# Optimization experiments

Measured on AMD Instinct MI355X. Metric: run time of the kernel, lower is better.

The kernel has to match this reference:

```python
import jax, jax.numpy as jnp
import numpy as np
import math

D_MODEL = 768
H = 12
D_FF = 3072
HEAD_DIM = D_MODEL // H
EPS = 1e-5


def setup_inputs() -> dict:
    key = jax.random.key(0)
    ks = jax.random.split(key, 12)
    s = 1.0 / math.sqrt(D_MODEL)
    inp = {
        "x": jax.random.normal(ks[0], (8, 1024, D_MODEL), dtype=jnp.float32),
        # attention projections (stored as [d_in, d_out])
        "wq": jax.random.normal(ks[1], (D_MODEL, D_MODEL), jnp.float32) * s,
        "bq": jnp.zeros((D_MODEL,), jnp.float32),
        "wk": jax.random.normal(ks[2], (D_MODEL, D_MODEL), jnp.float32) * s,
        "bk": jnp.zeros((D_MODEL,), jnp.float32),
        "wv": jax.random.normal(ks[3], (D_MODEL, D_MODEL), jnp.float32) * s,
        "bv": jnp.zeros((D_MODEL,), jnp.float32),
        "wo": jax.random.normal(ks[4], (D_MODEL, D_MODEL), jnp.float32) * s,
        "bo": jnp.zeros((D_MODEL,), jnp.float32),
        # FFN
        "w1": jax.random.normal(ks[5], (D_MODEL, D_FF), jnp.float32) * s,
        "b1": jnp.zeros((D_FF,), jnp.float32),
        "w2": jax.random.normal(ks[6], (D_FF, D_MODEL), jnp.float32) * (1.0 / math.sqrt(D_FF)),
        "b2": jnp.zeros((D_MODEL,), jnp.float32),
        # LayerNormalization scalar params (gemma/beta) for the two residual norms
        "g1": jnp.ones((1,), jnp.float32),
        "be1": jnp.zeros((1,), jnp.float32),
        "g2": jnp.ones((1,), jnp.float32),
        "be2": jnp.zeros((1,), jnp.float32),
    }
    return inp


def _layernorm(x, g, b):
    # torch: mean and UNBIASED std over last dim; divide by (std + eps)
    mean = jnp.mean(x, axis=-1, keepdims=True)
    std = jnp.std(x, axis=-1, keepdims=True, ddof=1)
    return g * (x - mean) / (std + EPS) + b


def _attention(x, wq, bq, wk, bk, wv, bv, wo, bo):
    B, N, _ = x.shape
    q = (x @ wq + bq).reshape(B, N, H, HEAD_DIM)
    k = (x @ wk + bk).reshape(B, N, H, HEAD_DIM)
    v = (x @ wv + bv).reshape(B, N, H, HEAD_DIM)
    scores = jnp.einsum("bqhd,bkhd->bhqk", q, k) / math.sqrt(HEAD_DIM)
    w = jax.nn.softmax(scores, axis=-1)
    out = jnp.einsum("bhqk,bkhd->bqhd", w, v).reshape(B, N, D_MODEL)
    return out @ wo + bo


def _ffn(x, w1, b1, w2, b2):
    return (jax.nn.gelu(x @ w1 + b1, approximate=False)) @ w2 + b2


def reference(x, wq, bq, wk, bk, wv, bv, wo, bo, w1, b1, w2, b2, g1, be1, g2, be2):
    # pre-LN residual block 1: attention
    x = x + _attention(_layernorm(x, g1, be1), wq, bq, wk, bk, wv, bv, wo, bo)
    # pre-LN residual block 2: FFN
    x = x + _ffn(_layernorm(x, g2, be2), w1, b1, w2, b2)
    return x
```

## Files before the change

### kernel.cpp

```cpp
#include <hip/hip_runtime.h>
#include <hip/hip_bf16.h>
#include <math.h>

typedef unsigned short u16;
typedef unsigned int u32;
typedef u16 u16x8 __attribute__((ext_vector_type(8)));
typedef __bf16 bf16x8 __attribute__((ext_vector_type(8)));
typedef float f32x4 __attribute__((ext_vector_type(4)));

#define MODE_GELU 1
#define MODE_RESF32 2
#define MODE_QKV 3

template <typename T, typename F>
__device__ __forceinline__ T bitcast(F f) { return __builtin_bit_cast(T, f); }

__device__ __forceinline__ u16 f2bf(float f) {
    unsigned int u = __float_as_uint(f);
    u = (u + 0x7fffu + ((u >> 16) & 1u)) >> 16;
    return (u16)u;
}

__device__ __forceinline__ u32 packbf(float lo, float hi) {
    return (u32)f2bf(lo) | ((u32)f2bf(hi) << 16);
}

__device__ __forceinline__ float fast_gelu(float x) {
    const float arg = x * (2.30220775f + 0.10294329f * x * x);
    const float e = exp2f(arg);
    return x * (1.0f - __builtin_amdgcn_rcpf(e + 1.0f));
}

__device__ __forceinline__ void gl_lds16(const u16* g, u16* l) {
    __builtin_amdgcn_global_load_lds(
        (const __attribute__((address_space(1))) unsigned int*)(const void*)g,
        (__attribute__((address_space(3))) unsigned int*)(void*)l,
        16, 0, 0);
}

__device__ __forceinline__ void stage64(const u16* __restrict__ src, int stride,
                                        u16* __restrict__ lds, int t)
{
    const int wave = t >> 6, lane = t & 63;
#pragma unroll
    for (int i = 0; i < 2; i++) {
        const int row = i * 32 + wave * 8 + (lane >> 3);
        const int s = lane & 7;
        const int f = (((row >> 3) & 1) << 2) | (row & 3);
        gl_lds16(src + (size_t)row * stride + (size_t)((s ^ f) << 3),
                 lds + i * 2048 + wave * 512);
    }
}

__global__ __launch_bounds__(256) void prep_kernel(
    const float* __restrict__ wq, const float* __restrict__ wk,
    const float* __restrict__ wv, const float* __restrict__ wo,
    const float* __restrict__ w1, const float* __restrict__ w2,
    const float* __restrict__ bq, const float* __restrict__ bk,
    const float* __restrict__ bv,
    u16* __restrict__ wqkvT, u16* __restrict__ woT,
    u16* __restrict__ w1T, u16* __restrict__ w2T, float* __restrict__ bqkv)
{
    const int blk = blockIdx.x;
    if (blk >= 6912) {
        const int t = (blk - 6912) * 256 + threadIdx.x;
        if (t < 2304)
            bqkv[t] = t < 768 ? bq[t] : (t < 1536 ? bk[t - 768] : bv[t - 1536]);
        return;
    }
    const float* W; u16* WT; int Krows, Ncols, lt;
    if (blk < 576)       { W = wq; WT = wqkvT;                       Krows = 768;  Ncols = 768;  lt = blk; }
    else if (blk < 1152) { W = wk; WT = wqkvT + (size_t)768 * 768;   Krows = 768;  Ncols = 768;  lt = blk - 576; }
    else if (blk < 1728) { W = wv; WT = wqkvT + (size_t)1536 * 768;  Krows = 768;  Ncols = 768;  lt = blk - 1152; }
    else if (blk < 2304) { W = wo; WT = woT;                         Krows = 768;  Ncols = 768;  lt = blk - 1728; }
    else if (blk < 4608) { W = w1; WT = w1T;                         Krows = 768;  Ncols = 3072; lt = blk - 2304; }
    else                 { W = w2; WT = w2T;                         Krows = 3072; Ncols = 768;  lt = blk - 4608; }
    const int ktiles = Krows >> 5;
    const int k0 = (lt % ktiles) * 32, n0 = (lt / ktiles) * 32;

    __shared__ float tile[32][33];
    const int tx = threadIdx.x & 31, ty = threadIdx.x >> 5;
#pragma unroll
    for (int j = 0; j < 32; j += 8)
        tile[ty + j][tx] = W[(size_t)(k0 + ty + j) * Ncols + n0 + tx];
    __syncthreads();
#pragma unroll
    for (int j = 0; j < 32; j += 8)
        WT[(size_t)(n0 + ty + j) * Krows + k0 + tx] = f2bf(tile[tx][ty + j]);
}

__global__ __launch_bounds__(256) void ln_kernel(
    const float* __restrict__ X, u16* __restrict__ Y,
    const float* __restrict__ gp, const float* __restrict__ bp)
{
    __shared__ float sbuf[8];
    const int row = blockIdx.x, t = threadIdx.x;
    const float* xr = X + (size_t)row * 768;
    float v0 = xr[t], v1 = xr[t + 256], v2 = xr[t + 512];
    float s = v0 + v1 + v2;
    float q = v0 * v0 + v1 * v1 + v2 * v2;
#pragma unroll
    for (int m = 1; m < 64; m <<= 1) {
        s += __shfl_xor(s, m, 64);
        q += __shfl_xor(q, m, 64);
    }
    const int wave = t >> 6, lane = t & 63;
    if (lane == 0) { sbuf[wave] = s; sbuf[4 + wave] = q; }
    __syncthreads();
    s = sbuf[0] + sbuf[1] + sbuf[2] + sbuf[3];
    q = sbuf[4] + sbuf[5] + sbuf[6] + sbuf[7];
    const float mean = s * (1.0f / 768.0f);
    float ssd = q - 768.0f * mean * mean;
    ssd = fmaxf(ssd, 0.0f);
    const float stdv = sqrtf(ssd * (1.0f / 767.0f));
    const float scale = gp[0] / (stdv + 1e-5f);
    const float beta = bp[0];
    u16* yr = Y + (size_t)row * 768;
    yr[t]       = f2bf((v0 - mean) * scale + beta);
    yr[t + 256] = f2bf((v1 - mean) * scale + beta);
    yr[t + 512] = f2bf((v2 - mean) * scale + beta);
}

template <int MODE>
__global__ __launch_bounds__(256) void gemm_kernel(
    const u16* __restrict__ A, const u16* __restrict__ BT,
    const float* __restrict__ bias, const float* __restrict__ res,
    void* __restrict__ out0, void* __restrict__ out1, void* __restrict__ out2,
    int M, int N, int K)
{
    __shared__ u16 sh[2][2][128 * 64];
    u16* shp = &sh[0][0][0];
    const int t = threadIdx.x;
    const int lane = t & 63, wave = t >> 6;
    const int wr = wave >> 1, wc = wave & 1;
    const int g = lane >> 4, c = lane & 15;
    const int bm = blockIdx.x, bn = blockIdx.y;

    const int srow = wave * 32 + (lane >> 3);
    const int scol = (lane & 7) * 8;
    const u16* Ag = A + (size_t)(bm * 128 + srow) * K + scol;
    const u16* Bg = BT + (size_t)(bn * 128 + srow) * K + scol;

    f32x4 acc[4][4] = {};
    const int nk = K >> 6;

#define STAGE_AB(buf, k0)                                                     \
    {                                                                         \
        _Pragma("unroll")                                                     \
        for (int it = 0; it < 4; it++) {                                      \
            gl_lds16(Ag + (size_t)(it * 8) * K + (k0), &sh[buf][0][wave * 2048 + it * 512]); \
            gl_lds16(Bg + (size_t)(it * 8) * K + (k0), &sh[buf][1][wave * 2048 + it * 512]); \
        }                                                                     \
    }

    STAGE_AB(0, 0);
    __syncthreads();

    for (int ks = 0; ks < nk; ks++) {
        const int cur = ks & 1;
        if (ks + 1 < nk) STAGE_AB(cur ^ 1, (ks + 1) << 6);
        const u16* Asb = sh[cur][0];
        const u16* Bsb = sh[cur][1];
        __builtin_amdgcn_s_setprio(1);
#pragma unroll
        for (int kk = 0; kk < 2; kk++) {
            bf16x8 af[4], bfr[4];
#pragma unroll
            for (int m = 0; m < 4; m++)
                af[m] = *(const bf16x8*)&Asb[(wr * 64 + m * 16 + c) * 64 + kk * 32 + g * 8];
#pragma unroll
            for (int n = 0; n < 4; n++)
                bfr[n] = *(const bf16x8*)&Bsb[(wc * 64 + n * 16 + c) * 64 + kk * 32 + g * 8];
#pragma unroll
            for (int m = 0; m < 4; m++)
#pragma unroll
                for (int n = 0; n < 4; n++)
                    acc[m][n] = __builtin_amdgcn_mfma_f32_16x16x32_bf16(
                        af[m], bfr[n], acc[m][n], 0, 0, 0);
        }
        __builtin_amdgcn_s_setprio(0);
        __syncthreads();
    }
#undef STAGE_AB

    if constexpr (MODE == MODE_QKV) {
        if (bn >= 12) {
#pragma unroll
            for (int m = 0; m < 4; m++) {
#pragma unroll
                for (int n = 0; n < 4; n++) {
                    const int colL = wc * 64 + n * 16 + c;
                    const int rowLb = wr * 64 + m * 16 + 4 * g;
                    const float bv = bias[bn * 128 + colL];
                    const u32 x0 = packbf(acc[m][n][0] + bv, acc[m][n][1] + bv);
                    const u32 x1 = packbf(acc[m][n][2] + bv, acc[m][n][3] + bv);
                    const int elem = colL * 128 + (rowLb ^ ((colL & 15) << 3));
                    ((u32*)shp)[elem >> 1] = x0;
                    ((u32*)shp)[(elem >> 1) + 1] = x1;
                }
            }
            __syncthreads();
            const int bn_off = bn - 12;
            const int bb = bm >> 3, kvb = (bm & 7) * 128;
            const int j8 = (t & 7) * 8;
#pragma unroll
            for (int it = 0; it < 4; it++) {
                const int colL2 = it * 32 + (t >> 3);
                const int gcol = bn_off * 128 + colL2;
                const int hh = gcol >> 6, d = gcol & 63;
                const size_t obase = ((size_t)(bb * 12 + hh) << 16) + ((size_t)d << 10) + kvb;
                const int X = (colL2 & 15) << 3;
#pragma unroll
                for (int half = 0; half < 2; half++) {
                    const int rowL2 = half * 64 + j8;
                    const int elem = colL2 * 128 + (rowL2 ^ X);
                    *(u16x8*)((u16*)out2 + obase + rowL2) = *(const u16x8*)&shp[elem];
                }
            }
            return;
        }
    }

#pragma unroll
    for (int m = 0; m < 4; m++) {
        const int row = bm * 128 + wr * 64 + m * 16 + 4 * g;
#pragma unroll
        for (int n = 0; n < 4; n++) {
            const int col = bn * 128 + wc * 64 + n * 16 + c;
            const float bv = bias[col];
#pragma unroll
            for (int i = 0; i < 4; i++) {
                float v = acc[m][n][i] + bv;
                if constexpr (MODE == MODE_GELU) {
                    ((u16*)out0)[(size_t)(row + i) * N + col] = f2bf(fast_gelu(v));
                } else if constexpr (MODE == MODE_RESF32) {
                    const size_t idx = (size_t)(row + i) * N + col;
                    ((float*)out0)[idx] = v + res[idx];
                } else {
                    const int sect = (col >= 768) ? 1 : 0;
                    const int colm = col - sect * 768;
                    u16* dst = sect ? (u16*)out1 : (u16*)out0;
                    dst[(size_t)(row + i) * 768 + colm] = f2bf(v);
                }
            }
        }
    }
}

__global__ __launch_bounds__(256) void attn_kernel(
    const u16* __restrict__ Qg, const u16* __restrict__ Kg,
    const u16* __restrict__ Vt_g, u16* __restrict__ O)
{
    __shared__ u16 Kl[2][4096];
    __shared__ u16 Vl[2][4096];
    const int t = threadIdx.x, lane = t & 63, wave = t >> 6;
    const int g = lane >> 4, c = lane & 15;
    const int l = blockIdx.x;
    const int pos = l >> 3;
    const int bh = (l & 7) * 12 + (pos >> 3);
    const int qt = pos & 7;
    const int b = bh / 12, h = bh % 12;
    const size_t rowb = (size_t)b * 1024;
    const int q0 = qt * 128 + wave * 32;

    bf16x8 qa[2], qb[2];
    {
        const u16* qp = Qg + (rowb + q0 + c) * 768 + h * 64 + g * 8;
        u16x8 a0 = *(const u16x8*)qp;
        u16x8 a1 = *(const u16x8*)(qp + 32);
        u16x8 b0 = *(const u16x8*)(qp + 16 * 768);
        u16x8 b1 = *(const u16x8*)(qp + 16 * 768 + 32);
        bf16x8 va0, va1, vb0, vb1;
#pragma unroll
        for (int j = 0; j < 8; j++) {
            const float SC = 0.18033688011112042f;
            va0[j] = (__bf16)(__uint_as_float(((u32)a0[j]) << 16) * SC);
            va1[j] = (__bf16)(__uint_as_float(((u32)a1[j]) << 16) * SC);
            vb0[j] = (__bf16)(__uint_as_float(((u32)b0[j]) << 16) * SC);
            vb1[j] = (__bf16)(__uint_as_float(((u32)b1[j]) << 16) * SC);
        }
        qa[0] = va0; qa[1] = va1; qb[0] = vb0; qb[1] = vb1;
    }

    int kro[4], kxo[4], vro[4];
#pragma unroll
    for (int n = 0; n < 4; n++) {
        const int pr = ((n >> 1) << 5) + ((c >> 2) << 3) + ((n & 1) << 2) + (c & 3);
        kro[n] = pr << 6;
        kxo[n] = (((pr >> 3) & 1) << 2) | (pr & 3);
        vro[n] = (n * 16 + c) << 6;
    }
    const int vxo = (((c >> 3) & 1) << 2) | (c & 3);

    const u16* ksrc = Kg + rowb * 768 + h * 64;
    const u16* vsrc = Vt_g + (size_t)bh * 65536;

    float m0 = -1e30f, l0 = 0.f, m1 = -1e30f, l1 = 0.f;
    f32x4 oa[4] = {}, ob[4] = {};
    const int srcb = (lane & 48) | ((lane >> 2) & 12);

    stage64(ksrc, 768, Kl[0], t);
    stage64(vsrc, 1024, Vl[0], t);
    __syncthreads();

    for (int kvt = 0; kvt < 16; ++kvt) {
        const u16* Kc = Kl[kvt & 1];
        const u16* Vc = Vl[kvt & 1];
        if (kvt < 15) {
            stage64(ksrc + (size_t)(kvt + 1) * 64 * 768, 768, Kl[(kvt + 1) & 1], t);
            stage64(vsrc + (kvt + 1) * 64, 1024, Vl[(kvt + 1) & 1], t);
        }

        f32x4 s0[4] = {}, s1[4] = {};
#pragma unroll
        for (int n = 0; n < 4; n++) {
#pragma unroll
            for (int kk = 0; kk < 2; kk++) {
                const bf16x8 kf = *(const bf16x8*)&Kc[kro[n] + ((((kk << 2) + g) ^ kxo[n]) << 3)];
                s0[n] = __builtin_amdgcn_mfma_f32_16x16x32_bf16(kf, qa[kk], s0[n], 0, 0, 0);
                s1[n] = __builtin_amdgcn_mfma_f32_16x16x32_bf16(kf, qb[kk], s1[n], 0, 0, 0);
            }
        }

        bf16x8 pa00, pa01;
        {
            float t0 = fmaxf(fmaxf(s0[0][0], s0[0][1]), fmaxf(s0[0][2], s0[0][3]));
            float t1 = fmaxf(fmaxf(s0[1][0], s0[1][1]), fmaxf(s0[1][2], s0[1][3]));
            float t2 = fmaxf(fmaxf(s0[2][0], s0[2][1]), fmaxf(s0[2][2], s0[2][3]));
            float t3 = fmaxf(fmaxf(s0[3][0], s0[3][1]), fmaxf(s0[3][2], s0[3][3]));
            float mx = fmaxf(fmaxf(t0, t1), fmaxf(t2, t3));
            mx = fmaxf(mx, __shfl_xor(mx, 16, 64));
            mx = fmaxf(mx, __shfl_xor(mx, 32, 64));
            if (!__all(mx <= m0 + 8.0f)) {
                const float mn = fmaxf(m0, mx);
                const float rsc = exp2f(m0 - mn);
                m0 = mn; l0 *= rsc;
                f32x4 rq;
#pragma unroll
                for (int i = 0; i < 4; i++) rq[i] = __shfl(rsc, srcb + i, 64);
#pragma unroll
                for (int n = 0; n < 4; n++) oa[n] *= rq;
            }
            float r = 0.f;
#pragma unroll
            for (int n = 0; n < 4; n++)
#pragma unroll
                for (int i = 0; i < 4; i++) {
                    s0[n][i] = exp2f(s0[n][i] - m0);
                    r += s0[n][i];
                }
            r += __shfl_xor(r, 16, 64);
            r += __shfl_xor(r, 32, 64);
            l0 += r;
#pragma unroll
            for (int i = 0; i < 4; i++) {
                pa00[i] = (__bf16)s0[0][i]; pa00[4 + i] = (__bf16)s0[1][i];
                pa01[i] = (__bf16)s0[2][i]; pa01[4 + i] = (__bf16)s0[3][i];
            }
        }
        bf16x8 pa10, pa11;
        {
            float t0 = fmaxf(fmaxf(s1[0][0], s1[0][1]), fmaxf(s1[0][2], s1[0][3]));
            float t1 = fmaxf(fmaxf(s1[1][0], s1[1][1]), fmaxf(s1[1][2], s1[1][3]));
            float t2 = fmaxf(fmaxf(s1[2][0], s1[2][1]), fmaxf(s1[2][2], s1[2][3]));
            float t3 = fmaxf(fmaxf(s1[3][0], s1[3][1]), fmaxf(s1[3][2], s1[3][3]));
            float mx = fmaxf(fmaxf(t0, t1), fmaxf(t2, t3));
            mx = fmaxf(mx, __shfl_xor(mx, 16, 64));
            mx = fmaxf(mx, __shfl_xor(mx, 32, 64));
            if (!__all(mx <= m1 + 8.0f)) {
                const float mn = fmaxf(m1, mx);
                const float rsc = exp2f(m1 - mn);
                m1 = mn; l1 *= rsc;
                f32x4 rq;
#pragma unroll
                for (int i = 0; i < 4; i++) rq[i] = __shfl(rsc, srcb + i, 64);
#pragma unroll
                for (int n = 0; n < 4; n++) ob[n] *= rq;
            }
            float r = 0.f;
#pragma unroll
            for (int n = 0; n < 4; n++)
#pragma unroll
                for (int i = 0; i < 4; i++) {
                    s1[n][i] = exp2f(s1[n][i] - m1);
                    r += s1[n][i];
                }
            r += __shfl_xor(r, 16, 64);
            r += __shfl_xor(r, 32, 64);
            l1 += r;
#pragma unroll
            for (int i = 0; i < 4; i++) {
                pa10[i] = (__bf16)s1[0][i]; pa10[4 + i] = (__bf16)s1[1][i];
                pa11[i] = (__bf16)s1[2][i]; pa11[4 + i] = (__bf16)s1[3][i];
            }
        }

#pragma unroll
        for (int n = 0; n < 4; n++) {
#pragma unroll
            for (int kk = 0; kk < 2; kk++) {
                const bf16x8 vf = *(const bf16x8*)&Vc[vro[n] + ((((kk << 2) + g) ^ vxo) << 3)];
                oa[n] = __builtin_amdgcn_mfma_f32_16x16x32_bf16(kk ? pa01 : pa00, vf, oa[n], 0, 0, 0);
                ob[n] = __builtin_amdgcn_mfma_f32_16x16x32_bf16(kk ? pa11 : pa10, vf, ob[n], 0, 0, 0);
            }
        }
        __syncthreads();
    }

#pragma unroll
    for (int i = 0; i < 4; i++) {
        const float la = __shfl(l0, srcb + i, 64);
        const float lb = __shfl(l1, srcb + i, 64);
        const float ia_ = 1.0f / fmaxf(la, 1e-30f);
        const float ib_ = 1.0f / fmaxf(lb, 1e-30f);
        const size_t ra_ = rowb + q0 + 4 * g + i;
#pragma unroll
        for (int n = 0; n < 4; n++) {
            O[ra_ * 768 + h * 64 + n * 16 + c]        = f2bf(oa[n][i] * ia_);
            O[(ra_ + 16) * 768 + h * 64 + n * 16 + c] = f2bf(ob[n][i] * ib_);
        }
    }
}

extern "C" void kernel_launch(void* const* d_in, const int* in_sizes, int n_in,
                              void* d_out, int out_size, void* d_ws, size_t ws_size,
                              hipStream_t stream)
{
    const float* x   = (const float*)d_in[0];
    const float* wq  = (const float*)d_in[1];
    const float* bq  = (const float*)d_in[2];
    const float* wk  = (const float*)d_in[3];
    const float* bk  = (const float*)d_in[4];
    const float* wv  = (const float*)d_in[5];
    const float* bv  = (const float*)d_in[6];
    const float* wo  = (const float*)d_in[7];
    const float* bo  = (const float*)d_in[8];
    const float* w1  = (const float*)d_in[9];
    const float* b1  = (const float*)d_in[10];
    const float* w2  = (const float*)d_in[11];
    const float* b2  = (const float*)d_in[12];
    const float* g1  = (const float*)d_in[13];
    const float* be1 = (const float*)d_in[14];
    const float* g2  = (const float*)d_in[15];
    const float* be2 = (const float*)d_in[16];

    char* ws = (char*)d_ws;
    constexpr size_t O_WQKV = 0;
    constexpr size_t O_WO   = 3538944;
    constexpr size_t O_W1   = 4718592;
    constexpr size_t O_W2   = 9437184;
    constexpr size_t O_BQKV = 14155776;
    constexpr size_t O_XLN  = 14168064;
    constexpr size_t O_Q    = O_XLN + 12582912;
    constexpr size_t O_K    = O_Q + 12582912;
    constexpr size_t O_VT   = O_K + 12582912;
    constexpr size_t O_ATTN = O_VT + 12582912;
    constexpr size_t O_H    = O_ATTN + 12582912;
    constexpr size_t O_F    = O_XLN;
    constexpr size_t O_HLN  = O_ATTN;

    u16* wqkvT = (u16*)(ws + O_WQKV);
    u16* woT   = (u16*)(ws + O_WO);
    u16* w1T   = (u16*)(ws + O_W1);
    u16* w2T   = (u16*)(ws + O_W2);
    float* bqkv = (float*)(ws + O_BQKV);
    u16* xln   = (u16*)(ws + O_XLN);
    u16* Qb    = (u16*)(ws + O_Q);
    u16* Kb    = (u16*)(ws + O_K);
    u16* VTg   = (u16*)(ws + O_VT);
    u16* attnb = (u16*)(ws + O_ATTN);
    float* h   = (float*)(ws + O_H);
    u16* fb    = (u16*)(ws + O_F);
    u16* hln   = (u16*)(ws + O_HLN);

    dim3 blk(256);
    prep_kernel<<<6921, blk, 0, stream>>>(wq, wk, wv, wo, w1, w2, bq, bk, bv,
                                          wqkvT, woT, w1T, w2T, bqkv);
    ln_kernel<<<8192, blk, 0, stream>>>(x, xln, g1, be1);
    gemm_kernel<MODE_QKV><<<dim3(64, 18), blk, 0, stream>>>(
        xln, wqkvT, bqkv, nullptr, Qb, Kb, VTg, 8192, 2304, 768);
    attn_kernel<<<768, blk, 0, stream>>>(Qb, Kb, VTg, attnb);
    gemm_kernel<MODE_RESF32><<<dim3(64, 6), blk, 0, stream>>>(
        attnb, woT, bo, x, h, nullptr, nullptr, 8192, 768, 768);
    ln_kernel<<<8192, blk, 0, stream>>>(h, hln, g2, be2);
    gemm_kernel<MODE_GELU><<<dim3(64, 24), blk, 0, stream>>>(
        hln, w1T, b1, nullptr, fb, nullptr, nullptr, 8192, 3072, 768);
    gemm_kernel<MODE_RESF32><<<dim3(64, 6), blk, 0, stream>>>(
        fb, w2T, b2, h, (float*)d_out, nullptr, nullptr, 8192, 768, 3072);
}
```

Measured before the change: 277.3 us.

## Halve attention query tile per block, fuse first layernorm into prep kernel

The attention kernel now gives each wave 16 query rows instead of 32 and launches twice as many blocks. This raises parallelism and lowers register pressure, but each block must re-stage K/V for fewer queries, so the K/V traffic per query doubles. s_setprio is set around the MFMA loops. The first layernorm is merged into the weight prep kernel as extra blocks, which removes one launch.

```diff
diff --git a/kernel.cpp b/kernel.cpp
--- a/kernel.cpp
+++ b/kernel.cpp
@@ -59,9 +59,39 @@
     const float* __restrict__ bq, const float* __restrict__ bk,
     const float* __restrict__ bv,
     u16* __restrict__ wqkvT, u16* __restrict__ woT,
-    u16* __restrict__ w1T, u16* __restrict__ w2T, float* __restrict__ bqkv)
+    u16* __restrict__ w1T, u16* __restrict__ w2T, float* __restrict__ bqkv,
+    const float* __restrict__ X, u16* __restrict__ Y,
+    const float* __restrict__ gp, const float* __restrict__ bp)
 {
     const int blk = blockIdx.x;
+    if (blk >= 6921) {
+        __shared__ float sbuf[8];
+        const int row = blk - 6921, t = threadIdx.x;
+        const float* xr = X + (size_t)row * 768;
+        float v0 = xr[t], v1 = xr[t + 256], v2 = xr[t + 512];
+        float s = v0 + v1 + v2;
+        float q = v0 * v0 + v1 * v1 + v2 * v2;
+#pragma unroll
+        for (int m = 1; m < 64; m <<= 1) {
+            s += __shfl_xor(s, m, 64);
+            q += __shfl_xor(q, m, 64);
+        }
+        const int wave = t >> 6, lane = t & 63;
+        if (lane == 0) { sbuf[wave] = s; sbuf[4 + wave] = q; }
+        __syncthreads();
+        s = sbuf[0] + sbuf[1] + sbuf[2] + sbuf[3];
+        q = sbuf[4] + sbuf[5] + sbuf[6] + sbuf[7];
+        const float mean = s * (1.0f / 768.0f);
+        float ssd = fmaxf(q - 768.0f * mean * mean, 0.0f);
+        const float stdv = sqrtf(ssd * (1.0f / 767.0f));
+        const float scale = gp[0] / (stdv + 1e-5f);
+        const float beta = bp[0];
+        u16* yr = Y + (size_t)row * 768;
+        yr[t]       = f2bf((v0 - mean) * scale + beta);
+        yr[t + 256] = f2bf((v1 - mean) * scale + beta);
+        yr[t + 512] = f2bf((v2 - mean) * scale + beta);
+        return;
+    }
     if (blk >= 6912) {
         const int t = (blk - 6912) * 256 + threadIdx.x;
         if (t < 2304)
@@ -110,8 +140,7 @@
     s = sbuf[0] + sbuf[1] + sbuf[2] + sbuf[3];
     q = sbuf[4] + sbuf[5] + sbuf[6] + sbuf[7];
     const float mean = s * (1.0f / 768.0f);
-    float ssd = q - 768.0f * mean * mean;
-    ssd = fmaxf(ssd, 0.0f);
+    float ssd = fmaxf(q - 768.0f * mean * mean, 0.0f);
     const float stdv = sqrtf(ssd * (1.0f / 767.0f));
     const float scale = gp[0] / (stdv + 1e-5f);
     const float beta = bp[0];
@@ -257,29 +286,25 @@
     const int g = lane >> 4, c = lane & 15;
     const int l = blockIdx.x;
     const int pos = l >> 3;
-    const int bh = (l & 7) * 12 + (pos >> 3);
-    const int qt = pos & 7;
-    const int b = bh / 12, h = bh % 12;
+    const int b = l & 7, h = pos >> 4;
+    const int qt = pos & 15;
+    const int bh = b * 12 + h;
     const size_t rowb = (size_t)b * 1024;
-    const int q0 = qt * 128 + wave * 32;
-
-    bf16x8 qa[2], qb[2];
+    const int q0 = qt * 64 + wave * 16;
+
+    bf16x8 qa[2];
     {
         const u16* qp = Qg + (rowb + q0 + c) * 768 + h * 64 + g * 8;
         u16x8 a0 = *(const u16x8*)qp;
         u16x8 a1 = *(const u16x8*)(qp + 32);
-        u16x8 b0 = *(const u16x8*)(qp + 16 * 768);
-        u16x8 b1 = *(const u16x8*)(qp + 16 * 768 + 32);
-        bf16x8 va0, va1, vb0, vb1;
+        bf16x8 va0, va1;
 #pragma unroll
         for (int j = 0; j < 8; j++) {
             const float SC = 0.18033688011112042f;
             va0[j] = (__bf16)(__uint_as_float(((u32)a0[j]) << 16) * SC);
             va1[j] = (__bf16)(__uint_as_float(((u32)a1[j]) << 16) * SC);
-            vb0[j] = (__bf16)(__uint_as_float(((u32)b0[j]) << 16) * SC);
-            vb1[j] = (__bf16)(__uint_as_float(((u32)b1[j]) << 16) * SC);
-        }
-        qa[0] = va0; qa[1] = va1; qb[0] = vb0; qb[1] = vb1;
+        }
+        qa[0] = va0; qa[1] = va1;
     }
 
     int kro[4], kxo[4], vro[4];
@@ -295,8 +320,8 @@
     const u16* ksrc = Kg + rowb * 768 + h * 64;
     const u16* vsrc = Vt_g + (size_t)bh * 65536;
 
-    float m0 = -1e30f, l0 = 0.f, m1 = -1e30f, l1 = 0.f;
-    f32x4 oa[4] = {}, ob[4] = {};
+    float m0 = -1e30f, l0 = 0.f;
+    f32x4 oa[4] = {};
     const int srcb = (lane & 48) | ((lane >> 2) & 12);
 
     stage64(ksrc, 768, Kl[0], t);
@@ -311,16 +336,17 @@
             stage64(vsrc + (kvt + 1) * 64, 1024, Vl[(kvt + 1) & 1], t);
         }
 
-        f32x4 s0[4] = {}, s1[4] = {};
+        f32x4 s0[4] = {};
+        __builtin_amdgcn_s_setprio(1);
 #pragma unroll
         for (int n = 0; n < 4; n++) {
 #pragma unroll
             for (int kk = 0; kk < 2; kk++) {
                 const bf16x8 kf = *(const bf16x8*)&Kc[kro[n] + ((((kk << 2) + g) ^ kxo[n]) << 3)];
                 s0[n] = __builtin_amdgcn_mfma_f32_16x16x32_bf16(kf, qa[kk], s0[n], 0, 0, 0);
-                s1[n] = __builtin_amdgcn_mfma_f32_16x16x32_bf16(kf, qb[kk], s1[n], 0, 0, 0);
-            }
-        }
+            }
+        }
+        __builtin_amdgcn_s_setprio(0);
 
         bf16x8 pa00, pa01;
         {
@@ -358,67 +384,28 @@
                 pa01[i] = (__bf16)s0[2][i]; pa01[4 + i] = (__bf16)s0[3][i];
             }
         }
-        bf16x8 pa10, pa11;
-        {
-            float t0 = fmaxf(fmaxf(s1[0][0], s1[0][1]), fmaxf(s1[0][2], s1[0][3]));
-            float t1 = fmaxf(fmaxf(s1[1][0], s1[1][1]), fmaxf(s1[1][2], s1[1][3]));
-            float t2 = fmaxf(fmaxf(s1[2][0], s1[2][1]), fmaxf(s1[2][2], s1[2][3]));
-            float t3 = fmaxf(fmaxf(s1[3][0], s1[3][1]), fmaxf(s1[3][2], s1[3][3]));
-            float mx = fmaxf(fmaxf(t0, t1), fmaxf(t2, t3));
-            mx = fmaxf(mx, __shfl_xor(mx, 16, 64));
-            mx = fmaxf(mx, __shfl_xor(mx, 32, 64));
-            if (!__all(mx <= m1 + 8.0f)) {
-                const float mn = fmaxf(m1, mx);
-                const float rsc = exp2f(m1 - mn);
-                m1 = mn; l1 *= rsc;
-                f32x4 rq;
-#pragma unroll
-                for (int i = 0; i < 4; i++) rq[i] = __shfl(rsc, srcb + i, 64);
-#pragma unroll
-                for (int n = 0; n < 4; n++) ob[n] *= rq;
-            }
-            float r = 0.f;
-#pragma unroll
-            for (int n = 0; n < 4; n++)
-#pragma unroll
-                for (int i = 0; i < 4; i++) {
-                    s1[n][i] = exp2f(s1[n][i] - m1);
-                    r += s1[n][i];
-                }
-            r += __shfl_xor(r, 16, 64);
-            r += __shfl_xor(r, 32, 64);
-            l1 += r;
-#pragma unroll
-            for (int i = 0; i < 4; i++) {
-                pa10[i] = (__bf16)s1[0][i]; pa10[4 + i] = (__bf16)s1[1][i];
-                pa11[i] = (__bf16)s1[2][i]; pa11[4 + i] = (__bf16)s1[3][i];
-            }
-        }
-
+
+        __builtin_amdgcn_s_setprio(1);
 #pragma unroll
         for (int n = 0; n < 4; n++) {
 #pragma unroll
             for (int kk = 0; kk < 2; kk++) {
                 const bf16x8 vf = *(const bf16x8*)&Vc[vro[n] + ((((kk << 2) + g) ^ vxo) << 3)];
                 oa[n] = __builtin_amdgcn_mfma_f32_16x16x32_bf16(kk ? pa01 : pa00, vf, oa[n], 0, 0, 0);
-                ob[n] = __builtin_amdgcn_mfma_f32_16x16x32_bf16(kk ? pa11 : pa10, vf, ob[n], 0, 0, 0);
-            }
-        }
+            }
+        }
+        __builtin_amdgcn_s_setprio(0);
         __syncthreads();
     }
 
 #pragma unroll
     for (int i = 0; i < 4; i++) {
         const float la = __shfl(l0, srcb + i, 64);
-        const float lb = __shfl(l1, srcb + i, 64);
         const float ia_ = 1.0f / fmaxf(la, 1e-30f);
-        const float ib_ = 1.0f / fmaxf(lb, 1e-30f);
         const size_t ra_ = rowb + q0 + 4 * g + i;
 #pragma unroll
-        for (int n = 0; n < 4; n++) {
-            O[ra_ * 768 + h * 64 + n * 16 + c]        = f2bf(oa[n][i] * ia_);
-            O[(ra_ + 16) * 768 + h * 64 + n * 16 + c] = f2bf(ob[n][i] * ib_);
-        }
+        for (int n = 0; n < 4; n++)
+            O[ra_ * 768 + h * 64 + n * 16 + c] = f2bf(oa[n][i] * ia_);
     }
 }
 
@@ -474,12 +461,12 @@
     u16* hln   = (u16*)(ws + O_HLN);
 
     dim3 blk(256);
-    prep_kernel<<<6921, blk, 0, stream>>>(wq, wk, wv, wo, w1, w2, bq, bk, bv,
-                                          wqkvT, woT, w1T, w2T, bqkv);
-    ln_kernel<<<8192, blk, 0, stream>>>(x, xln, g1, be1);
+    prep_kernel<<<6921 + 8192, blk, 0, stream>>>(wq, wk, wv, wo, w1, w2, bq, bk, bv,
+                                                 wqkvT, woT, w1T, w2T, bqkv,
+                                                 x, xln, g1, be1);
     gemm_kernel<MODE_QKV><<<dim3(64, 18), blk, 0, stream>>>(
         xln, wqkvT, bqkv, nullptr, Qb, Kb, VTg, 8192, 2304, 768);
-    attn_kernel<<<768, blk, 0, stream>>>(Qb, Kb, VTg, attnb);
+    attn_kernel<<<1536, blk, 0, stream>>>(Qb, Kb, VTg, attnb);
     gemm_kernel<MODE_RESF32><<<dim3(64, 6), blk, 0, stream>>>(
         attnb, woT, bo, x, h, nullptr, nullptr, 8192, 768, 768);
     ln_kernel<<<8192, blk, 0, stream>>>(h, hln, g2, be2);
```

Result: faster. 269.0 us (-3.0%).
